# Optimization experiments

Measured on AMD Instinct MI355X. Metric: run time of the kernel, lower is better.

The kernel has to match this reference:

```python
import jax, jax.numpy as jnp
import numpy as np

NUM_WORDS = 32000
EMB_DIM = 512
HALF_H = 512  # hidden_size // 2 per direction
L, B = 128, 64


def _lstm_cell(x, h, c, Wih, Whh, b):
    # PyTorch LSTMCell: gates = x@Wih^T + h@Whh^T + (bih+bhh), gate order i,f,g,o
    gates = x @ Wih.T + h @ Whh.T + b  # [B, 4H]
    i, f, g, o = jnp.split(gates, 4, axis=-1)
    c_new = jax.nn.sigmoid(f) * c + jax.nn.sigmoid(i) * jnp.tanh(g)
    h_new = jax.nn.sigmoid(o) * jnp.tanh(c_new)
    return h_new, c_new


def _run_lstm(emb, mask, Wih, Whh, b, reverse):
    Bd = emb.shape[1]
    H = Whh.shape[1]

    def step(carry, inp):
        h, c = carry
        x, m = inp
        h2, c2 = _lstm_cell(x, h, c, Wih, Whh, b)
        h2 = h2 * m[:, None]  # zero state at padded positions (as in source)
        c2 = c2 * m[:, None]
        return (h2, c2), h2

    init = (jnp.zeros((Bd, H), emb.dtype), jnp.zeros((Bd, H), emb.dtype))
    _, hs = jax.lax.scan(step, init, (emb, mask), reverse=reverse)
    return hs  # [L, B, H]


def setup_inputs() -> dict:
    key = jax.random.key(0)
    ks = jax.random.split(key, 12)
    lengths = jax.random.randint(ks[0], (B,), L // 2, L + 1)
    mask = (jnp.arange(L)[:, None] < lengths[None, :]).astype(jnp.float32)  # [L, B]
    data = jax.random.randint(ks[1], (L, B), 0, NUM_WORDS)
    data = jnp.where(mask == 0, -1, data)  # padding value is -1
    stdv = 1.0 / np.sqrt(HALF_H)

    def u(k, shape):
        return jax.random.uniform(k, shape, jnp.float32, -stdv, stdv)

    return {
        "data": data,
        "mask": mask,
        "emb_table": jax.random.normal(ks[2], (NUM_WORDS + 1, EMB_DIM), jnp.float32) * 0.02,
        "Wih_f": u(ks[3], (4 * HALF_H, EMB_DIM)),
        "Whh_f": u(ks[4], (4 * HALF_H, HALF_H)),
        "bih_f": u(ks[5], (4 * HALF_H,)),
        "bhh_f": u(ks[6], (4 * HALF_H,)),
        "Wih_b": u(ks[7], (4 * HALF_H, EMB_DIM)),
        "Whh_b": u(ks[8], (4 * HALF_H, HALF_H)),
        "bih_b": u(ks[9], (4 * HALF_H,)),
        "bhh_b": u(ks[10], (4 * HALF_H,)),
    }


def reference(data, mask, emb_table, Wih_f, Whh_f, bih_f, bhh_f, Wih_b, Whh_b, bih_b, bhh_b):
    # q = data + (data == -1) * (num_words + 1)  ->  padding index == num_words
    q = jnp.where(data == -1, NUM_WORDS, data)
    emb = emb_table[q]  # [L, B, E]
    emb = jnp.where((q == NUM_WORDS)[..., None], jnp.zeros((), emb.dtype), emb)
    hs_f = _run_lstm(emb, mask, Wih_f, Whh_f, bih_f + bhh_f, reverse=False)
    hs_b = _run_lstm(emb, mask, Wih_b, Whh_b, bih_b + bhh_b, reverse=True)
    return jnp.concatenate([hs_f, hs_b], axis=-1)  # [L, B, hidden_size]
```

## Files before the change

### kernel.cpp

```cpp
#include <hip/hip_runtime.h>


typedef float  f32x4  __attribute__((ext_vector_type(4)));
typedef __bf16 bf16x8 __attribute__((ext_vector_type(8)));
typedef __bf16 bf16;

#define HB_OFF   ((size_t)0)
#define FLAG_OFF ((size_t)262144)
#define XF_OFF   ((size_t)264192)
#define WS_ZERO_BYTES ((size_t)266240)
#define XP_OFF   ((size_t)266240)
#define XP_BYTES ((size_t)134217728)
#define EBF_OFF  (XP_OFF + XP_BYTES)
#define EBF_BYTES ((size_t)8388608)
#define WS_NEED  (EBF_OFF + EBF_BYTES)

__device__ __forceinline__ float sigmoidf_(float x) {
    return 1.0f / (1.0f + __expf(-x));
}
__device__ __forceinline__ float tanhf_(float x) {
    return 2.0f * sigmoidf_(2.0f * x) - 1.0f;
}
__device__ __forceinline__ bf16x8 cvt8(const float* p) {
    float4 a = *(const float4*)p;
    float4 b = *(const float4*)(p + 4);
    bf16x8 r;
    r[0] = (bf16)a.x; r[1] = (bf16)a.y; r[2] = (bf16)a.z; r[3] = (bf16)a.w;
    r[4] = (bf16)b.x; r[5] = (bf16)b.y; r[6] = (bf16)b.z; r[7] = (bf16)b.w;
    return r;
}
__device__ __forceinline__ bf16x8 cvt8v(uint4 u0, uint4 u1) {
    float4 a = __builtin_bit_cast(float4, u0);
    float4 b = __builtin_bit_cast(float4, u1);
    bf16x8 r;
    r[0] = (bf16)a.x; r[1] = (bf16)a.y; r[2] = (bf16)a.z; r[3] = (bf16)a.w;
    r[4] = (bf16)b.x; r[5] = (bf16)b.y; r[6] = (bf16)b.z; r[7] = (bf16)b.w;
    return r;
}
__device__ __forceinline__ void store4_sc1(float* p, f32x4 v) {
    asm volatile("global_store_dwordx4 %0, %1, off sc1"
                 :: "v"((unsigned long long)p), "v"(v) : "memory");
}
__device__ __forceinline__ void wait_xf(unsigned long long a) {
    for (;;) {
        unsigned v;
        asm volatile("global_load_ushort %0, %1, off sc1\n\t"
                     "s_waitcnt vmcnt(0)"
                     : "=&v"(v) : "v"(a) : "memory");
        if (v != 0) break;
        __builtin_amdgcn_s_sleep(2);
    }
}

__global__ __launch_bounds__(256) void init_ws_legacy(unsigned long long* __restrict__ w) {
    const size_t i = (size_t)blockIdx.x * 256 + threadIdx.x;
    if (i < WS_ZERO_BYTES / 8) w[i] = 0ull;
}

__global__ __launch_bounds__(256) void emb_gather(
    const int* __restrict__ data, const float* __restrict__ table,
    bf16* __restrict__ ebf, unsigned long long* __restrict__ wz)
{
    const int bid = blockIdx.x, tid = threadIdx.x;
    if (bid < 130) {
        wz[(size_t)bid * 256 + tid] = 0ull;
    }
    const int wave = tid >> 6, lane = tid & 63;
    const int rr = bid * 4 + wave;
    const int qv = data[rr];
    bf16x8 v;
    if (qv >= 0) {
        v = cvt8(table + (size_t)qv * 512 + lane * 8);
    } else {
#pragma unroll
        for (int i = 0; i < 8; ++i) v[i] = (bf16)0.f;
    }
    *(bf16x8*)(ebf + (size_t)rr * 512 + lane * 8) = v;
}

__global__ __launch_bounds__(256, 1) void fused_scan(
    const float* __restrict__ mask,
    const float* __restrict__ whh_f, const float* __restrict__ whh_b,
    const float* __restrict__ bih_f, const float* __restrict__ bhh_f,
    const float* __restrict__ bih_b, const float* __restrict__ bhh_b,
    const float* __restrict__ wih_f, const float* __restrict__ wih_b,
    const bf16* __restrict__ ebf,
    float* __restrict__ xp,
    bf16* __restrict__ hbuf,
    unsigned* __restrict__ flags,
    unsigned short* __restrict__ xf,
    float* __restrict__ out)
{
    __shared__ bf16 sM[4096 * 8];

    const int tid = threadIdx.x, bid = blockIdx.x;
    const int wave = tid >> 6, lane = tid & 63;
    const int c = lane & 15, q = lane >> 4;

    if (bid >= 128) {
        const int xbid = bid - 128;
        const int dir = xbid >> 9, cc = (xbid >> 4) & 31, sh = xbid & 15;
        const float* wih = dir ? wih_b : wih_f;

        for (int e = tid; e < 4096; e += 256) {
            const int ec = e & 15, eq = (e >> 4) & 3, et = (e >> 6) & 3, ekc = e >> 8;
            const int kbx = 2 * cc + (et >> 1), t4x = et & 1;
            const size_t orig = (size_t)((ec & 3) * 512 + kbx * 8 + 2 * (ec >> 2) + t4x);
            *(bf16x8*)(&sM[e * 8]) = cvt8(&wih[orig * 512 + ekc * 32 + eq * 8]);
        }
        __syncthreads();

        const int hrow = 16 * wave + c;
        const f32x4 zz = {0.f, 0.f, 0.f, 0.f};
        const size_t flin = (size_t)wave * 512 + (q * 16 + c) * 8;

        for (int s0 = 0; s0 < 8; ++s0) {
            const int s = sh * 8 + s0;
            const int tt = dir ? (127 - s) : s;
            const bf16* arow = ebf + (size_t)(tt * 64 + hrow) * 512;
            uint4 af[16];
#pragma unroll
            for (int kc = 0; kc < 16; ++kc)
                af[kc] = *(const uint4*)(arow + kc * 32 + q * 8);

            f32x4 acc0 = zz, acc1 = zz, acc2 = zz, acc3 = zz;
#pragma unroll
            for (int kc = 0; kc < 16; ++kc) {
                const bf16x8 a = __builtin_bit_cast(bf16x8, af[kc]);
                acc0 = __builtin_amdgcn_mfma_f32_16x16x32_bf16(
                    a, *(const bf16x8*)(&sM[(kc * 256 +   0 + q * 16 + c) * 8]), acc0, 0, 0, 0);
                acc1 = __builtin_amdgcn_mfma_f32_16x16x32_bf16(
                    a, *(const bf16x8*)(&sM[(kc * 256 +  64 + q * 16 + c) * 8]), acc1, 0, 0, 0);
                acc2 = __builtin_amdgcn_mfma_f32_16x16x32_bf16(
                    a, *(const bf16x8*)(&sM[(kc * 256 + 128 + q * 16 + c) * 8]), acc2, 0, 0, 0);
                acc3 = __builtin_amdgcn_mfma_f32_16x16x32_bf16(
                    a, *(const bf16x8*)(&sM[(kc * 256 + 192 + q * 16 + c) * 8]), acc3, 0, 0, 0);
            }
            const size_t r0 = ((size_t)(dir * 64 + 2 * cc)     * 128 + s) * 2048 + flin;
            const size_t r1 = ((size_t)(dir * 64 + 2 * cc + 1) * 128 + s) * 2048 + flin;
            store4_sc1(&xp[r0],     acc0);
            store4_sc1(&xp[r0 + 4], acc1);
            store4_sc1(&xp[r1],     acc2);
            store4_sc1(&xp[r1 + 4], acc3);
        }
        __builtin_amdgcn_s_waitcnt(0x0F70);
        __syncthreads();
        if (tid == 0) {
            const unsigned long long fa =
                (unsigned long long)&xf[(dir * 32 + cc) * 16 + sh];
            asm volatile("global_store_short %0, %1, off sc1"
                         :: "v"(fa), "v"(1u) : "memory");
        }
        return;
    }

    const int dir = bid >> 6, kb = bid & 63;
    const int g = c & 3;

    const float* whh = dir ? whh_b : whh_f;
    const float* bih = dir ? bih_b : bih_f;
    const float* bhh = dir ? bhh_b : bhh_f;

    for (int e = tid; e < 2048; e += 256) {
        const int ec = e & 15, eq = (e >> 4) & 3, et = (e >> 6) & 1, ekc = e >> 7;
        const size_t orig = (size_t)((ec & 3) * 512 + kb * 8 + 2 * (ec >> 2) + et);
        *(bf16x8*)(&sM[e * 8]) = cvt8(&whh[orig * 512 + ekc * 32 + eq * 8]);
    }
    float bias_v[2];
#pragma unroll
    for (int t4 = 0; t4 < 2; ++t4) {
        const int orig = g * 512 + kb * 8 + 2 * (c >> 2) + t4;
        bias_v[t4] = bih[orig] + bhh[orig];
    }

    float cst[2][4] = {{0.f, 0.f, 0.f, 0.f}, {0.f, 0.f, 0.f, 0.f}};
    const int hrow = 16 * wave + c;
    const int myflag = dir * 256 + wave * 64 + kb;
    const int fidx   = dir * 256 + wave * 64 + lane;
    const f32x4 zz = {0.f, 0.f, 0.f, 0.f};
    __syncthreads();

    const unsigned long long xfb =
        (unsigned long long)(xf + ((size_t)(dir * 32 + (kb >> 1)) * 16));

    const float* xpb = xp + (size_t)bid * 128 * 2048
                          + (size_t)wave * 512 + (q * 16 + c) * 8;
    wait_xf(xfb);
    float4 xq0, xq1;
    {
        uint4 u0, u1;
        const unsigned long long xa = (unsigned long long)xpb;
        asm volatile("global_load_dwordx4 %0, %2, off sc1\n\t"
                     "global_load_dwordx4 %1, %2, off offset:16 sc1\n\t"
                     "s_waitcnt vmcnt(0)"
                     : "=&v"(u0), "=&v"(u1) : "v"(xa) : "memory");
        xq0 = __builtin_bit_cast(float4, u0);
        xq1 = __builtin_bit_cast(float4, u1);
    }
    float4 mv;
    {
        const int tt0 = dir ? 127 : 0;
        mv = *(const float4*)(&mask[tt0 * 64 + 16 * wave + 4 * q]);
    }

    for (int s = 0; s < 128; ++s) {
        const int tt = dir ? (127 - s) : s;

        const unsigned tgt = (unsigned)s;
        unsigned fa = __hip_atomic_load(flags + fidx, __ATOMIC_RELAXED, __HIP_MEMORY_SCOPE_AGENT);
        unsigned fb = __hip_atomic_load(flags + fidx, __ATOMIC_RELAXED, __HIP_MEMORY_SCOPE_AGENT);
        for (;;) {
            if (__all(fa >= tgt)) break;
            fa = fb;
            fb = __hip_atomic_load(flags + fidx, __ATOMIC_RELAXED, __HIP_MEMORY_SCOPE_AGENT);
        }
        __asm__ volatile("" ::: "memory");

        const bf16* hb = hbuf + (size_t)(dir * 2 + (s & 1)) * (64 * 512);
        bf16*       hw = hbuf + (size_t)(dir * 2 + ((s + 1) & 1)) * (64 * 512);

        const unsigned long long ha =
            (unsigned long long)hb + (unsigned)(hrow * 1024 + q * 16);
        uint4 af[16];
        asm volatile(
            "global_load_dwordx4 %0,  %16, off sc1\n\t"
            "global_load_dwordx4 %1,  %16, off offset:64   sc1\n\t"
            "global_load_dwordx4 %2,  %16, off offset:128  sc1\n\t"
            "global_load_dwordx4 %3,  %16, off offset:192  sc1\n\t"
            "global_load_dwordx4 %4,  %16, off offset:256  sc1\n\t"
            "global_load_dwordx4 %5,  %16, off offset:320  sc1\n\t"
            "global_load_dwordx4 %6,  %16, off offset:384  sc1\n\t"
            "global_load_dwordx4 %7,  %16, off offset:448  sc1\n\t"
            "global_load_dwordx4 %8,  %16, off offset:512  sc1\n\t"
            "global_load_dwordx4 %9,  %16, off offset:576  sc1\n\t"
            "global_load_dwordx4 %10, %16, off offset:640  sc1\n\t"
            "global_load_dwordx4 %11, %16, off offset:704  sc1\n\t"
            "global_load_dwordx4 %12, %16, off offset:768  sc1\n\t"
            "global_load_dwordx4 %13, %16, off offset:832  sc1\n\t"
            "global_load_dwordx4 %14, %16, off offset:896  sc1\n\t"
            "global_load_dwordx4 %15, %16, off offset:960  sc1\n\t"
            "s_waitcnt vmcnt(0)"
            : "=&v"(af[0]),  "=&v"(af[1]),  "=&v"(af[2]),  "=&v"(af[3]),
              "=&v"(af[4]),  "=&v"(af[5]),  "=&v"(af[6]),  "=&v"(af[7]),
              "=&v"(af[8]),  "=&v"(af[9]),  "=&v"(af[10]), "=&v"(af[11]),
              "=&v"(af[12]), "=&v"(af[13]), "=&v"(af[14]), "=&v"(af[15])
            : "v"(ha)
            : "memory");

        f32x4 acc0 = zz, acc1 = zz;
#pragma unroll
        for (int kc = 0; kc < 16; ++kc) {
            const bf16x8 a  = __builtin_bit_cast(bf16x8, af[kc]);
            const bf16x8 b0 = *(const bf16x8*)(&sM[(kc * 128 + q * 16 + c) * 8]);
            const bf16x8 b1 = *(const bf16x8*)(&sM[(kc * 128 + 64 + q * 16 + c) * 8]);
            acc0 = __builtin_amdgcn_mfma_f32_16x16x32_bf16(a, b0, acc0, 0, 0, 0);
            acc1 = __builtin_amdgcn_mfma_f32_16x16x32_bf16(a, b1, acc1, 0, 0, 0);
        }

        unsigned* hw32 = (unsigned*)hw;
        float hreg[4][2];
#pragma unroll
        for (int r = 0; r < 4; ++r) {
            const int b_ = 16 * wave + 4 * q + r;
            const float m = (&mv.x)[r];
            float hv01[2];
#pragma unroll
            for (int t4 = 0; t4 < 2; ++t4) {
                float v = (t4 ? acc1[r] : acc0[r])
                        + (t4 ? (&xq1.x)[r] : (&xq0.x)[r]) + bias_v[t4];
                const float v1 = __shfl_xor(v, 1);
                const float v2 = __shfl_xor(v, 2);
                const float v3 = __shfl_xor(v, 3);
                const float gi = (g == 0) ? v  : (g == 1) ? v1 : (g == 2) ? v2 : v3;
                const float gf = (g == 0) ? v1 : (g == 1) ? v  : (g == 2) ? v3 : v2;
                const float gG = (g == 0) ? v2 : (g == 1) ? v3 : (g == 2) ? v  : v1;
                const float go = (g == 0) ? v3 : (g == 1) ? v2 : (g == 2) ? v1 : v;
                const float cn = sigmoidf_(gf) * cst[t4][r] + sigmoidf_(gi) * tanhf_(gG);
                float hv       = sigmoidf_(go) * tanhf_(cn);
                cst[t4][r] = cn * m;
                hv *= m;
                hv01[t4] = hv;
            }
            hreg[r][0] = hv01[0]; hreg[r][1] = hv01[1];
            if (g == 0) {
                const unsigned u =
                    (unsigned)__builtin_bit_cast(unsigned short, (bf16)hv01[0]) |
                    ((unsigned)__builtin_bit_cast(unsigned short, (bf16)hv01[1]) << 16);
                __hip_atomic_store(hw32 + b_ * 256 + kb * 4 + (c >> 2), u,
                                   __ATOMIC_RELAXED, __HIP_MEMORY_SCOPE_AGENT);
            }
        }

        __asm__ volatile("" ::: "memory");
        __builtin_amdgcn_s_waitcnt(0x0F70);
        if (lane == 0)
            __hip_atomic_store(flags + myflag, (unsigned)(s + 1),
                               __ATOMIC_RELAXED, __HIP_MEMORY_SCOPE_AGENT);

        if (g == 0) {
            const int j2 = dir * 512 + kb * 8 + 2 * (c >> 2);
#pragma unroll
            for (int r = 0; r < 4; ++r) {
                const int b_ = 16 * wave + 4 * q + r;
                float2 o2; o2.x = hreg[r][0]; o2.y = hreg[r][1];
                *(float2*)(&out[(size_t)(tt * 64 + b_) * 1024 + j2]) = o2;
            }
        }
        if (s < 127) {
            if (((s + 1) & 7) == 0)
                wait_xf(xfb + (unsigned)(((s + 1) >> 3) * 2));
            uint4 u0, u1;
            const unsigned long long xa =
                (unsigned long long)(xpb + (size_t)(s + 1) * 2048);
            asm volatile("global_load_dwordx4 %0, %2, off sc1\n\t"
                         "global_load_dwordx4 %1, %2, off offset:16 sc1\n\t"
                         "s_waitcnt vmcnt(0)"
                         : "=&v"(u0), "=&v"(u1) : "v"(xa) : "memory");
            xq0 = __builtin_bit_cast(float4, u0);
            xq1 = __builtin_bit_cast(float4, u1);
            const int tt_n = dir ? (126 - s) : (s + 1);
            mv  = *(const float4*)(&mask[tt_n * 64 + 16 * wave + 4 * q]);
        }
    }
}

__global__ __launch_bounds__(256, 1) void lstm_scan_legacy(
    const int*   __restrict__ data,
    const float* __restrict__ mask,
    const float* __restrict__ table,
    const float* __restrict__ wih_f, const float* __restrict__ whh_f,
    const float* __restrict__ bih_f, const float* __restrict__ bhh_f,
    const float* __restrict__ wih_b, const float* __restrict__ whh_b,
    const float* __restrict__ bih_b, const float* __restrict__ bhh_b,
    bf16* __restrict__ hbuf,
    unsigned* __restrict__ flags,
    const float* __restrict__ zrow,
    float* __restrict__ out)
{
    __shared__ bf16 sW[2048 * 8];
    __shared__ bf16 sV[2048 * 8];

    const int tid = threadIdx.x, bid = blockIdx.x;
    const int dir = bid >> 6, kb = bid & 63;
    const int wave = tid >> 6, lane = tid & 63;
    const int c = lane & 15, q = lane >> 4, g = c & 3;

    const float* wih = dir ? wih_b : wih_f;
    const float* whh = dir ? whh_b : whh_f;
    const float* bih = dir ? bih_b : bih_f;
    const float* bhh = dir ? bhh_b : bhh_f;

    for (int e = tid; e < 2048; e += 256) {
        const int ec = e & 15, eq = (e >> 4) & 3, et = (e >> 6) & 1, ekc = e >> 7;
        const size_t orig = (size_t)((ec & 3) * 512 + kb * 8 + 2 * (ec >> 2) + et);
        const size_t off = orig * 512 + ekc * 32 + eq * 8;
        *(bf16x8*)(&sW[e * 8]) = cvt8(&whh[off]);
        *(bf16x8*)(&sV[e * 8]) = cvt8(&wih[off]);
    }
    float bias_v[2];
#pragma unroll
    for (int t4 = 0; t4 < 2; ++t4) {
        const int orig = g * 512 + kb * 8 + 2 * (c >> 2) + t4;
        bias_v[t4] = bih[orig] + bhh[orig];
    }

    float cst[2][4] = {{0.f, 0.f, 0.f, 0.f}, {0.f, 0.f, 0.f, 0.f}};
    const int hrow = 16 * wave + c;
    const int myflag = dir * 256 + kb * 4 + wave;
    const int fbase = dir * 256;
    const f32x4 zz = {0.f, 0.f, 0.f, 0.f};
    __syncthreads();

    uint4 xe[32];
    float4 mv;
    int qv_n;
    {
        const int tt0 = dir ? 127 : 0;
        const int qv0 = data[tt0 * 64 + hrow];
        mv = *(const float4*)(&mask[tt0 * 64 + 16 * wave + 4 * q]);
        const float* erow = (qv0 >= 0) ? (table + (size_t)qv0 * 512) : zrow;
#pragma unroll
        for (int kc = 0; kc < 16; ++kc) {
            xe[2 * kc]     = *(const uint4*)(erow + kc * 32 + q * 8);
            xe[2 * kc + 1] = *(const uint4*)(erow + kc * 32 + q * 8 + 4);
        }
        const int tt1 = dir ? 126 : 1;
        qv_n = data[tt1 * 64 + hrow];
    }

    for (int s = 0; s < 128; ++s) {
        const int tt = dir ? (127 - s) : s;

        f32x4 accx0 = zz, accx1 = zz;
#pragma unroll
        for (int kc = 0; kc < 16; ++kc) {
            const bf16x8 e  = cvt8v(xe[2 * kc], xe[2 * kc + 1]);
            const bf16x8 b0 = *(const bf16x8*)(&sV[(kc * 128 + q * 16 + c) * 8]);
            const bf16x8 b1 = *(const bf16x8*)(&sV[(kc * 128 + 64 + q * 16 + c) * 8]);
            accx0 = __builtin_amdgcn_mfma_f32_16x16x32_bf16(e, b0, accx0, 0, 0, 0);
            accx1 = __builtin_amdgcn_mfma_f32_16x16x32_bf16(e, b1, accx1, 0, 0, 0);
        }

        const unsigned tgt = (unsigned)s;
        for (;;) {
            const unsigned a0 = __hip_atomic_load(flags + fbase + lane,       __ATOMIC_RELAXED, __HIP_MEMORY_SCOPE_AGENT);
            const unsigned a1 = __hip_atomic_load(flags + fbase + 64  + lane, __ATOMIC_RELAXED, __HIP_MEMORY_SCOPE_AGENT);
            const unsigned a2 = __hip_atomic_load(flags + fbase + 128 + lane, __ATOMIC_RELAXED, __HIP_MEMORY_SCOPE_AGENT);
            const unsigned a3 = __hip_atomic_load(flags + fbase + 192 + lane, __ATOMIC_RELAXED, __HIP_MEMORY_SCOPE_AGENT);
            if (__all(a0 >= tgt && a1 >= tgt && a2 >= tgt && a3 >= tgt)) break;
            __builtin_amdgcn_s_sleep(1);
        }
        __asm__ volatile("" ::: "memory");

        const bf16* hb = hbuf + (size_t)(dir * 2 + (s & 1)) * (64 * 512);
        bf16*       hw = hbuf + (size_t)(dir * 2 + ((s + 1) & 1)) * (64 * 512);

        const unsigned long long ha =
            (unsigned long long)hb + (unsigned)(hrow * 1024 + q * 16);
        uint4 af[16];
        asm volatile(
            "global_load_dwordx4 %0,  %16, off sc1\n\t"
            "global_load_dwordx4 %1,  %16, off offset:64   sc1\n\t"
            "global_load_dwordx4 %2,  %16, off offset:128  sc1\n\t"
            "global_load_dwordx4 %3,  %16, off offset:192  sc1\n\t"
            "global_load_dwordx4 %4,  %16, off offset:256  sc1\n\t"
            "global_load_dwordx4 %5,  %16, off offset:320  sc1\n\t"
            "global_load_dwordx4 %6,  %16, off offset:384  sc1\n\t"
            "global_load_dwordx4 %7,  %16, off offset:448  sc1\n\t"
            "global_load_dwordx4 %8,  %16, off offset:512  sc1\n\t"
            "global_load_dwordx4 %9,  %16, off offset:576  sc1\n\t"
            "global_load_dwordx4 %10, %16, off offset:640  sc1\n\t"
            "global_load_dwordx4 %11, %16, off offset:704  sc1\n\t"
            "global_load_dwordx4 %12, %16, off offset:768  sc1\n\t"
            "global_load_dwordx4 %13, %16, off offset:832  sc1\n\t"
            "global_load_dwordx4 %14, %16, off offset:896  sc1\n\t"
            "global_load_dwordx4 %15, %16, off offset:960  sc1\n\t"
            "s_waitcnt vmcnt(0)"
            : "=&v"(af[0]),  "=&v"(af[1]),  "=&v"(af[2]),  "=&v"(af[3]),
              "=&v"(af[4]),  "=&v"(af[5]),  "=&v"(af[6]),  "=&v"(af[7]),
              "=&v"(af[8]),  "=&v"(af[9]),  "=&v"(af[10]), "=&v"(af[11]),
              "=&v"(af[12]), "=&v"(af[13]), "=&v"(af[14]), "=&v"(af[15])
            : "v"(ha)
            : "memory");

        f32x4 acc0 = zz, acc1 = zz;
#pragma unroll
        for (int kc = 0; kc < 16; ++kc) {
            const bf16x8 a  = __builtin_bit_cast(bf16x8, af[kc]);
            const bf16x8 b0 = *(const bf16x8*)(&sW[(kc * 128 + q * 16 + c) * 8]);
            const bf16x8 b1 = *(const bf16x8*)(&sW[(kc * 128 + 64 + q * 16 + c) * 8]);
            acc0 = __builtin_amdgcn_mfma_f32_16x16x32_bf16(a, b0, acc0, 0, 0, 0);
            acc1 = __builtin_amdgcn_mfma_f32_16x16x32_bf16(a, b1, acc1, 0, 0, 0);
        }

        unsigned* hw32 = (unsigned*)hw;
        float hreg[4][2];
#pragma unroll
        for (int r = 0; r < 4; ++r) {
            const int b_ = 16 * wave + 4 * q + r;
            const float m = (&mv.x)[r];
            float hv01[2];
#pragma unroll
            for (int t4 = 0; t4 < 2; ++t4) {
                float v = (t4 ? acc1[r] : acc0[r]) + (t4 ? accx1[r] : accx0[r]) + bias_v[t4];
                const float v1 = __shfl_xor(v, 1);
                const float v2 = __shfl_xor(v, 2);
                const float v3 = __shfl_xor(v, 3);
                const float gi = (g == 0) ? v  : (g == 1) ? v1 : (g == 2) ? v2 : v3;
                const float gf = (g == 0) ? v1 : (g == 1) ? v  : (g == 2) ? v3 : v2;
                const float gG = (g == 0) ? v2 : (g == 1) ? v3 : (g == 2) ? v  : v1;
                const float go = (g == 0) ? v3 : (g == 1) ? v2 : (g == 2) ? v1 : v;
                const float cn = sigmoidf_(gf) * cst[t4][r] + sigmoidf_(gi) * tanhf_(gG);
                float hv       = sigmoidf_(go) * tanhf_(cn);
                cst[t4][r] = cn * m;
                hv *= m;
                hv01[t4] = hv;
            }
            hreg[r][0] = hv01[0]; hreg[r][1] = hv01[1];
            if (g == 0) {
                const unsigned u =
                    (unsigned)__builtin_bit_cast(unsigned short, (bf16)hv01[0]) |
                    ((unsigned)__builtin_bit_cast(unsigned short, (bf16)hv01[1]) << 16);
                __hip_atomic_store(hw32 + b_ * 256 + kb * 4 + (c >> 2), u,
                                   __ATOMIC_RELAXED, __HIP_MEMORY_SCOPE_AGENT);
            }
        }

        __asm__ volatile("" ::: "memory");
        __builtin_amdgcn_s_waitcnt(0x0F70);
        if (lane == 0)
            __hip_atomic_store(flags + myflag, (unsigned)(s + 1),
                               __ATOMIC_RELAXED, __HIP_MEMORY_SCOPE_AGENT);

        if (g == 0) {
            const int j2 = dir * 512 + kb * 8 + 2 * (c >> 2);
#pragma unroll
            for (int r = 0; r < 4; ++r) {
                const int b_ = 16 * wave + 4 * q + r;
                float2 o2; o2.x = hreg[r][0]; o2.y = hreg[r][1];
                *(float2*)(&out[(size_t)(tt * 64 + b_) * 1024 + j2]) = o2;
            }
        }
        if (s < 127) {
            const int tt_n = dir ? (126 - s) : (s + 1);
            const float* erow = (qv_n >= 0) ? (table + (size_t)qv_n * 512) : zrow;
#pragma unroll
            for (int kc = 0; kc < 16; ++kc) {
                xe[2 * kc]     = *(const uint4*)(erow + kc * 32 + q * 8);
                xe[2 * kc + 1] = *(const uint4*)(erow + kc * 32 + q * 8 + 4);
            }
            mv = *(const float4*)(&mask[tt_n * 64 + 16 * wave + 4 * q]);
            if (s < 126) {
                const int tt_n2 = dir ? (125 - s) : (s + 2);
                qv_n = data[tt_n2 * 64 + hrow];
            }
        }
    }
}

extern "C" void kernel_launch(void* const* d_in, const int* in_sizes, int n_in,
                              void* d_out, int out_size, void* d_ws, size_t ws_size,
                              hipStream_t stream) {
    const int*   data  = (const int*)d_in[0];
    const float* mask  = (const float*)d_in[1];
    const float* table = (const float*)d_in[2];
    const float* wih_f = (const float*)d_in[3];
    const float* whh_f = (const float*)d_in[4];
    const float* bih_f = (const float*)d_in[5];
    const float* bhh_f = (const float*)d_in[6];
    const float* wih_b = (const float*)d_in[7];
    const float* whh_b = (const float*)d_in[8];
    const float* bih_b = (const float*)d_in[9];
    const float* bhh_b = (const float*)d_in[10];
    float* outp = (float*)d_out;

    char* ws = (char*)d_ws;
    bf16*     hbuf  = (bf16*)(ws + HB_OFF);
    unsigned* flagp = (unsigned*)(ws + FLAG_OFF);

    if (ws_size >= WS_NEED) {
        bf16*  ebf = (bf16*)(ws + EBF_OFF);
        float* xp  = (float*)(ws + XP_OFF);
        unsigned short* xf = (unsigned short*)(ws + XF_OFF);
        emb_gather<<<2048, 256, 0, stream>>>(data, table, ebf,
                                             (unsigned long long*)ws);
        fused_scan<<<1152, 256, 0, stream>>>(mask, whh_f, whh_b,
                                             bih_f, bhh_f, bih_b, bhh_b,
                                             wih_f, wih_b, ebf, xp,
                                             hbuf, flagp, xf, outp);
    } else {
        const float* zrow = (const float*)(ws + XF_OFF);
        init_ws_legacy<<<(int)((WS_ZERO_BYTES / 8 + 255) / 256), 256, 0, stream>>>(
            (unsigned long long*)ws);
        lstm_scan_legacy<<<128, 256, 0, stream>>>(data, mask, table,
                                                  wih_f, whh_f, bih_f, bhh_f,
                                                  wih_b, whh_b, bih_b, bhh_b,
                                                  hbuf, flagp, zrow, outp);
    }
}
```

Baseline: 1.016 ms.

## Halve recurrent-scan blocks, give each block 16 hidden units per direction

```diff
diff --git a/kernel.cpp b/kernel.cpp
--- a/kernel.cpp
+++ b/kernel.cpp
@@ -97,22 +97,22 @@
     const int wave = tid >> 6, lane = tid & 63;
     const int c = lane & 15, q = lane >> 4;
 
-    if (bid >= 128) {
-        const int xbid = bid - 128;
-        const int dir = xbid >> 9, cc = (xbid >> 4) & 31, sh = xbid & 15;
+    if (bid >= 64) {
+        const int xbid = bid - 64;
+        const int dir = xbid >> 9, kb = (xbid >> 4) & 31, sh = xbid & 15;
         const float* wih = dir ? wih_b : wih_f;
 
         for (int e = tid; e < 4096; e += 256) {
             const int ec = e & 15, eq = (e >> 4) & 3, et = (e >> 6) & 3, ekc = e >> 8;
-            const int kbx = 2 * cc + (et >> 1), t4x = et & 1;
-            const size_t orig = (size_t)((ec & 3) * 512 + kbx * 8 + 2 * (ec >> 2) + t4x);
+            const size_t orig = (size_t)((ec & 3) * 512 + kb * 16 + 4 * (ec >> 2) + et);
             *(bf16x8*)(&sM[e * 8]) = cvt8(&wih[orig * 512 + ekc * 32 + eq * 8]);
         }
         __syncthreads();
 
         const int hrow = 16 * wave + c;
         const f32x4 zz = {0.f, 0.f, 0.f, 0.f};
-        const size_t flin = (size_t)wave * 512 + (q * 16 + c) * 8;
+        float* xpB = xp + ((size_t)(dir * 32 + kb) * 128) * 4096
+                   + (size_t)(wave * 64 + lane) * 16;
 
         for (int s0 = 0; s0 < 8; ++s0) {
             const int s = sh * 8 + s0;
@@ -136,66 +136,70 @@
                 acc3 = __builtin_amdgcn_mfma_f32_16x16x32_bf16(
                     a, *(const bf16x8*)(&sM[(kc * 256 + 192 + q * 16 + c) * 8]), acc3, 0, 0, 0);
             }
-            const size_t r0 = ((size_t)(dir * 64 + 2 * cc)     * 128 + s) * 2048 + flin;
-            const size_t r1 = ((size_t)(dir * 64 + 2 * cc + 1) * 128 + s) * 2048 + flin;
-            store4_sc1(&xp[r0],     acc0);
-            store4_sc1(&xp[r0 + 4], acc1);
-            store4_sc1(&xp[r1],     acc2);
-            store4_sc1(&xp[r1 + 4], acc3);
+            float* dst = xpB + (size_t)s * 4096;
+            store4_sc1(dst,      acc0);
+            store4_sc1(dst + 4,  acc1);
+            store4_sc1(dst + 8,  acc2);
+            store4_sc1(dst + 12, acc3);
         }
         __builtin_amdgcn_s_waitcnt(0x0F70);
         __syncthreads();
         if (tid == 0) {
             const unsigned long long fa =
-                (unsigned long long)&xf[(dir * 32 + cc) * 16 + sh];
+                (unsigned long long)&xf[(dir * 32 + kb) * 16 + sh];
             asm volatile("global_store_short %0, %1, off sc1"
                          :: "v"(fa), "v"(1u) : "memory");
         }
         return;
     }
 
-    const int dir = bid >> 6, kb = bid & 63;
+    const int dir = bid >> 5, kb = bid & 31;
     const int g = c & 3;
 
     const float* whh = dir ? whh_b : whh_f;
     const float* bih = dir ? bih_b : bih_f;
     const float* bhh = dir ? bhh_b : bhh_f;
 
-    for (int e = tid; e < 2048; e += 256) {
-        const int ec = e & 15, eq = (e >> 4) & 3, et = (e >> 6) & 1, ekc = e >> 7;
-        const size_t orig = (size_t)((ec & 3) * 512 + kb * 8 + 2 * (ec >> 2) + et);
+    for (int e = tid; e < 4096; e += 256) {
+        const int ec = e & 15, eq = (e >> 4) & 3, et = (e >> 6) & 3, ekc = e >> 8;
+        const size_t orig = (size_t)((ec & 3) * 512 + kb * 16 + 4 * (ec >> 2) + et);
         *(bf16x8*)(&sM[e * 8]) = cvt8(&whh[orig * 512 + ekc * 32 + eq * 8]);
     }
-    float bias_v[2];
-#pragma unroll
-    for (int t4 = 0; t4 < 2; ++t4) {
-        const int orig = g * 512 + kb * 8 + 2 * (c >> 2) + t4;
-        bias_v[t4] = bih[orig] + bhh[orig];
-    }
-
-    float cst[2][4] = {{0.f, 0.f, 0.f, 0.f}, {0.f, 0.f, 0.f, 0.f}};
+    float bias_v[4];
+#pragma unroll
+    for (int t = 0; t < 4; ++t) {
+        const int orig = g * 512 + kb * 16 + 4 * (c >> 2) + t;
+        bias_v[t] = bih[orig] + bhh[orig];
+    }
+
+    float cst[4][4] = {{0,0,0,0},{0,0,0,0},{0,0,0,0},{0,0,0,0}};
     const int hrow = 16 * wave + c;
-    const int myflag = dir * 256 + wave * 64 + kb;
-    const int fidx   = dir * 256 + wave * 64 + lane;
+    const int myflag = dir * 128 + wave * 32 + kb;
+    const int fidx   = dir * 128 + wave * 32 + (lane & 31);
     const f32x4 zz = {0.f, 0.f, 0.f, 0.f};
     __syncthreads();
 
     const unsigned long long xfb =
-        (unsigned long long)(xf + ((size_t)(dir * 32 + (kb >> 1)) * 16));
-
-    const float* xpb = xp + (size_t)bid * 128 * 2048
-                          + (size_t)wave * 512 + (q * 16 + c) * 8;
+        (unsigned long long)(xf + ((size_t)(dir * 32 + kb) * 16));
+
+    const float* xpb = xp + ((size_t)(dir * 32 + kb) * 128) * 4096
+                     + (size_t)(wave * 64 + lane) * 16;
     wait_xf(xfb);
-    float4 xq0, xq1;
+    float4 xq[4];
     {
-        uint4 u0, u1;
+        uint4 u0, u1, u2, u3;
         const unsigned long long xa = (unsigned long long)xpb;
-        asm volatile("global_load_dwordx4 %0, %2, off sc1\n\t"
-                     "global_load_dwordx4 %1, %2, off offset:16 sc1\n\t"
+        asm volatile("global_load_dwordx4 %0, %4, off sc1\n\t"
+                     "global_load_dwordx4 %1, %4, off offset:16 sc1\n\t"
+                     "global_load_dwordx4 %2, %4, off offset:32 sc1\n\t"
+                     "global_load_dwordx4 %3, %4, off offset:48 sc1\n\t"
                      "s_waitcnt vmcnt(0)"
-                     : "=&v"(u0), "=&v"(u1) : "v"(xa) : "memory");
-        xq0 = __builtin_bit_cast(float4, u0);
-        xq1 = __builtin_bit_cast(float4, u1);
+                     : "=&v"(u0), "=&v"(u1), "=&v"(u2), "=&v"(u3)
+                     : "v"(xa) : "memory");
+        xq[0] = __builtin_bit_cast(float4, u0);
+        xq[1] = __builtin_bit_cast(float4, u1);
+        xq[2] = __builtin_bit_cast(float4, u2);
+        xq[3] = __builtin_bit_cast(float4, u3);
     }
     float4 mv;
     {
@@ -207,12 +211,10 @@
         const int tt = dir ? (127 - s) : s;
 
         const unsigned tgt = (unsigned)s;
-        unsigned fa = __hip_atomic_load(flags + fidx, __ATOMIC_RELAXED, __HIP_MEMORY_SCOPE_AGENT);
-        unsigned fb = __hip_atomic_load(flags + fidx, __ATOMIC_RELAXED, __HIP_MEMORY_SCOPE_AGENT);
         for (;;) {
+            const unsigned fa = __hip_atomic_load(flags + fidx, __ATOMIC_RELAXED,
+                                                  __HIP_MEMORY_SCOPE_AGENT);
             if (__all(fa >= tgt)) break;
-            fa = fb;
-            fb = __hip_atomic_load(flags + fidx, __ATOMIC_RELAXED, __HIP_MEMORY_SCOPE_AGENT);
         }
         __asm__ volatile("" ::: "memory");
 
@@ -247,27 +249,25 @@
             : "v"(ha)
             : "memory");
 
-        f32x4 acc0 = zz, acc1 = zz;
+        f32x4 acc[4] = {zz, zz, zz, zz};
 #pragma unroll
         for (int kc = 0; kc < 16; ++kc) {
-            const bf16x8 a  = __builtin_bit_cast(bf16x8, af[kc]);
-            const bf16x8 b0 = *(const bf16x8*)(&sM[(kc * 128 + q * 16 + c) * 8]);
-            const bf16x8 b1 = *(const bf16x8*)(&sM[(kc * 128 + 64 + q * 16 + c) * 8]);
-            acc0 = __builtin_amdgcn_mfma_f32_16x16x32_bf16(a, b0, acc0, 0, 0, 0);
-            acc1 = __builtin_amdgcn_mfma_f32_16x16x32_bf16(a, b1, acc1, 0, 0, 0);
-        }
-
-        unsigned* hw32 = (unsigned*)hw;
-        float hreg[4][2];
+            const bf16x8 a = __builtin_bit_cast(bf16x8, af[kc]);
+#pragma unroll
+            for (int t = 0; t < 4; ++t) {
+                const bf16x8 b = *(const bf16x8*)(&sM[(kc * 256 + t * 64 + q * 16 + c) * 8]);
+                acc[t] = __builtin_amdgcn_mfma_f32_16x16x32_bf16(a, b, acc[t], 0, 0, 0);
+            }
+        }
+
+        float hstore[4][4];
 #pragma unroll
         for (int r = 0; r < 4; ++r) {
             const int b_ = 16 * wave + 4 * q + r;
             const float m = (&mv.x)[r];
-            float hv01[2];
-#pragma unroll
-            for (int t4 = 0; t4 < 2; ++t4) {
-                float v = (t4 ? acc1[r] : acc0[r])
-                        + (t4 ? (&xq1.x)[r] : (&xq0.x)[r]) + bias_v[t4];
+#pragma unroll
+            for (int t = 0; t < 4; ++t) {
+                float v = acc[t][r] + (&xq[t].x)[r] + bias_v[t];
                 const float v1 = __shfl_xor(v, 1);
                 const float v2 = __shfl_xor(v, 2);
                 const float v3 = __shfl_xor(v, 3);
@@ -275,19 +275,25 @@
                 const float gf = (g == 0) ? v1 : (g == 1) ? v  : (g == 2) ? v3 : v2;
                 const float gG = (g == 0) ? v2 : (g == 1) ? v3 : (g == 2) ? v  : v1;
                 const float go = (g == 0) ? v3 : (g == 1) ? v2 : (g == 2) ? v1 : v;
-                const float cn = sigmoidf_(gf) * cst[t4][r] + sigmoidf_(gi) * tanhf_(gG);
+                const float cn = sigmoidf_(gf) * cst[t][r] + sigmoidf_(gi) * tanhf_(gG);
                 float hv       = sigmoidf_(go) * tanhf_(cn);
-                cst[t4][r] = cn * m;
+                cst[t][r] = cn * m;
                 hv *= m;
-                hv01[t4] = hv;
-            }
-            hreg[r][0] = hv01[0]; hreg[r][1] = hv01[1];
+                hstore[r][t] = hv;
+            }
             if (g == 0) {
-                const unsigned u =
-                    (unsigned)__builtin_bit_cast(unsigned short, (bf16)hv01[0]) |
-                    ((unsigned)__builtin_bit_cast(unsigned short, (bf16)hv01[1]) << 16);
-                __hip_atomic_store(hw32 + b_ * 256 + kb * 4 + (c >> 2), u,
-                                   __ATOMIC_RELAXED, __HIP_MEMORY_SCOPE_AGENT);
+                const unsigned lo =
+                    (unsigned)__builtin_bit_cast(unsigned short, (bf16)hstore[r][0]) |
+                    ((unsigned)__builtin_bit_cast(unsigned short, (bf16)hstore[r][1]) << 16);
+                const unsigned hi =
+                    (unsigned)__builtin_bit_cast(unsigned short, (bf16)hstore[r][2]) |
+                    ((unsigned)__builtin_bit_cast(unsigned short, (bf16)hstore[r][3]) << 16);
+                const unsigned long long du =
+                    (unsigned long long)lo | ((unsigned long long)hi << 32);
+                const unsigned long long da = (unsigned long long)hw
+                    + (unsigned)(b_ * 1024 + kb * 32 + (c >> 2) * 8);
+                asm volatile("global_store_dwordx2 %0, %1, off sc1"
+                             :: "v"(da), "v"(du) : "memory");
             }
         }
 
@@ -298,26 +304,33 @@
                                __ATOMIC_RELAXED, __HIP_MEMORY_SCOPE_AGENT);
 
         if (g == 0) {
-            const int j2 = dir * 512 + kb * 8 + 2 * (c >> 2);
+            const int j2 = dir * 512 + kb * 16 + 4 * (c >> 2);
 #pragma unroll
             for (int r = 0; r < 4; ++r) {
                 const int b_ = 16 * wave + 4 * q + r;
-                float2 o2; o2.x = hreg[r][0]; o2.y = hreg[r][1];
-                *(float2*)(&out[(size_t)(tt * 64 + b_) * 1024 + j2]) = o2;
+                float4 o4;
+                o4.x = hstore[r][0]; o4.y = hstore[r][1];
+                o4.z = hstore[r][2]; o4.w = hstore[r][3];
+                *(float4*)(&out[(size_t)(tt * 64 + b_) * 1024 + j2]) = o4;
             }
         }
         if (s < 127) {
             if (((s + 1) & 7) == 0)
                 wait_xf(xfb + (unsigned)(((s + 1) >> 3) * 2));
-            uint4 u0, u1;
+            uint4 u0, u1, u2, u3;
             const unsigned long long xa =
-                (unsigned long long)(xpb + (size_t)(s + 1) * 2048);
-            asm volatile("global_load_dwordx4 %0, %2, off sc1\n\t"
-                         "global_load_dwordx4 %1, %2, off offset:16 sc1\n\t"
+                (unsigned long long)(xpb + (size_t)(s + 1) * 4096);
+            asm volatile("global_load_dwordx4 %0, %4, off sc1\n\t"
+                         "global_load_dwordx4 %1, %4, off offset:16 sc1\n\t"
+                         "global_load_dwordx4 %2, %4, off offset:32 sc1\n\t"
+                         "global_load_dwordx4 %3, %4, off offset:48 sc1\n\t"
                          "s_waitcnt vmcnt(0)"
-                         : "=&v"(u0), "=&v"(u1) : "v"(xa) : "memory");
-            xq0 = __builtin_bit_cast(float4, u0);
-            xq1 = __builtin_bit_cast(float4, u1);
+                         : "=&v"(u0), "=&v"(u1), "=&v"(u2), "=&v"(u3)
+                         : "v"(xa) : "memory");
+            xq[0] = __builtin_bit_cast(float4, u0);
+            xq[1] = __builtin_bit_cast(float4, u1);
+            xq[2] = __builtin_bit_cast(float4, u2);
+            xq[3] = __builtin_bit_cast(float4, u3);
             const int tt_n = dir ? (126 - s) : (s + 1);
             mv  = *(const float4*)(&mask[tt_n * 64 + 16 * wave + 4 * q]);
         }
@@ -544,7 +557,7 @@
         unsigned short* xf = (unsigned short*)(ws + XF_OFF);
         emb_gather<<<2048, 256, 0, stream>>>(data, table, ebf,
                                              (unsigned long long*)ws);
-        fused_scan<<<1152, 256, 0, stream>>>(mask, whh_f, whh_b,
+        fused_scan<<<1088, 256, 0, stream>>>(mask, whh_f, whh_b,
                                              bih_f, bhh_f, bih_b, bhh_b,
                                              wih_f, wih_b, ebf, xp,
                                              hbuf, flagp, xf, outp);
```

New measurement: 1.209 ms. +19.1%, slower.
